# Optimization experiments

Measured on AMD Instinct MI355X. Metric: run time of the kernel, lower is better.

## Reference

```python
import jax, jax.numpy as jnp
import numpy as np

N, E, G, IN, H, L, C = 20000, 320000, 128, 16, 64, 4, 10
AVG_D_LOG = float(np.log(17.0))  # log(avg_degree + 1)


def setup_inputs() -> dict:
    key = jax.random.key(0)
    ks = jax.random.split(key, 24)
    p = lambda k, shape: jax.random.normal(k, shape, dtype=jnp.float32) * 0.05
    return dict(
        h=jax.random.normal(ks[0], (N, IN), jnp.float32),
        snorm_n=jax.random.uniform(ks[1], (N, 1), jnp.float32, 0.05, 1.0),
        embW=p(ks[2], (IN, H)), embB=p(ks[3], (H,)),
        preW=p(ks[4], (L, 2 * H, H)), preB=p(ks[5], (L, H)),
        postW=p(ks[6], (L, 13 * H, H)), postB=p(ks[7], (L, H)),
        mixW=p(ks[8], (L, H, H)), mixB=p(ks[9], (L, H)),
        r1W=p(ks[10], (H, H // 2)), r1B=p(ks[11], (H // 2,)),
        r2W=p(ks[12], (H // 2, H // 4)), r2B=p(ks[13], (H // 4,)),
        r3W=p(ks[14], (H // 4, C)), r3B=p(ks[15], (C,)),
        src=jax.random.randint(ks[16], (E,), 0, N),
        dst=jax.random.randint(ks[17], (E,), 0, N),
        graph_ids=jnp.sort(jax.random.randint(ks[18], (N,), 0, G)),
    )


def _pna_forward(h, snorm_n, embW, embB, preW, preB, postW, postB, mixW, mixB,
                 r1W, r1B, r2W, r2B, r3W, r3B, src, dst, graph_ids):
    # Degree-based scalers (computed once; graph is fixed across layers)
    deg = jax.ops.segment_sum(jnp.ones((E,), h.dtype), dst, num_segments=N)  # [N]
    degc = jnp.maximum(deg, 1.0)[:, None]
    logd = jnp.log(deg + 1.0)
    amp = (logd / AVG_D_LOG)[:, None]                      # amplification scaler
    att = (AVG_D_LOG / jnp.maximum(logd, 1e-5))[:, None]   # attenuation scaler
    has_nb = (deg > 0.0)[:, None]

    x = h @ embW + embB  # node embedding [N, H]
    for i in range(L):
        x_in = x
        # pretrans: per-edge message from cat(h_src, h_dst)  [E, H]
        m = jnp.concatenate([x[src], x[dst]], axis=-1) @ preW[i] + preB[i]
        # multi-aggregator reduce at dst: mean, max, min, std
        mean = jax.ops.segment_sum(m, dst, num_segments=N) / degc
        msq = jax.ops.segment_sum(m * m, dst, num_segments=N) / degc
        std = jnp.sqrt(jax.nn.relu(msq - mean * mean) + 1e-5)
        mx = jnp.where(has_nb, jax.ops.segment_max(m, dst, num_segments=N), 0.0)
        mn = jnp.where(has_nb, jax.ops.segment_min(m, dst, num_segments=N), 0.0)
        agg = jnp.concatenate([mean, mx, mn, std], axis=-1)  # [N, 4H]
        # degree scalers: identity, amplification, attenuation -> [N, 12H]
        scaled = jnp.concatenate([agg, agg * amp, agg * att], axis=-1)
        # posttrans over cat(scaled_agg, h) -> [N, H]
        y = jnp.concatenate([scaled, x], axis=-1) @ postW[i] + postB[i]
        # tower mixing network (LeakyReLU FC)
        y = jax.nn.leaky_relu(y @ mixW[i] + mixB[i])
        y = y * snorm_n          # graph norm
        x = x_in + y             # residual
    # mean-nodes readout per graph
    gsum = jax.ops.segment_sum(x, graph_ids, num_segments=G)
    cnt = jnp.maximum(jax.ops.segment_sum(jnp.ones((N,), x.dtype), graph_ids, num_segments=G), 1.0)
    hg = gsum / cnt[:, None]
    # MLPReadout: two halving ReLU layers + classifier
    hg = jax.nn.relu(hg @ r1W + r1B)
    hg = jax.nn.relu(hg @ r2W + r2B)
    return hg @ r3W + r3B  # [G, C]


def reference(h, snorm_n, embW, embB, preW, preB, postW, postB, mixW, mixB,
              r1W, r1B, r2W, r2B, r3W, r3B, src, dst, graph_ids):
    return _pna_forward(h, snorm_n, embW, embB, preW, preB, postW, postB,
                        mixW, mixB, r1W, r1B, r2W, r2B, r3W, r3B,
                        src, dst, graph_ids)
```

## Files before the change

### kernel.cpp

```cpp
#include <hip/hip_runtime.h>
#include <math.h>

#define N_ 20000
#define E_ 320000
#define G_ 128
#define IN_ 16
#define H_ 64
#define L_ 4
#define C_ 10
#define AVG_D_LOG 2.8332133440562162f

union F4 { float4 v; float f[4]; };

typedef _Float16 h8 __attribute__((ext_vector_type(8)));
typedef _Float16 h4 __attribute__((ext_vector_type(4)));
typedef float f4x __attribute__((ext_vector_type(4)));
#define MFMA16(a, b, c) __builtin_amdgcn_mfma_f32_16x16x32_f16((a), (b), (c), 0, 0, 0)


__global__ __launch_bounds__(256) void k_setup(
    const float* __restrict__ h, const float* __restrict__ embW, const float* __restrict__ embB,
    float* __restrict__ x,
    const float* __restrict__ preW, const float* __restrict__ postW, const float* __restrict__ mixW,
    _Float16* __restrict__ preWT, _Float16* __restrict__ postWT, _Float16* __restrict__ mixWT,
    int* __restrict__ zbase) {
  int bb = blockIdx.x, tid = threadIdx.x;
  if (bb < 5000) {
    int n = bb * 4 + (tid >> 6);
    int c = tid & 63;
    float acc = embB[c];
#pragma unroll
    for (int k = 0; k < IN_; k++) acc += h[n * IN_ + k] * embW[k * H_ + c];
    x[n * H_ + c] = acc;
  } else if (bb < 6024) {
    int idx = (bb - 5000) * 256 + tid;
    if (idx < 32768) {
      int l = idx >> 13, r = idx & 8191;
      int c = r >> 6, k = r & 63;
      preWT[idx] = (_Float16)preW[l * 8192 + k * 64 + c];
    } else if (idx < 245760) {
      int j = idx - 32768;
      int l = j / 53248, r = j % 53248;
      int c = r / 832, k = r % 832;
      postWT[j] = (_Float16)postW[l * 53248 + k * 64 + c];
    } else {
      int j = idx - 245760;
      int l = j >> 12, r = j & 4095;
      int c = r >> 6, k = r & 63;
      mixWT[j] = (_Float16)mixW[l * 4096 + k * 64 + c];
    }
  } else {
    int i = (bb - 6024) * 256 + tid;
    if (i < 2 * N_) zbase[i] = 0;
  }
}


__global__ __launch_bounds__(256) void k_hist(const int* __restrict__ dst, int* __restrict__ deg) {
  int e = blockIdx.x * 256 + threadIdx.x;
  if (e < E_) atomicAdd(&deg[dst[e]], 1);
}

__global__ __launch_bounds__(1024) void k_scan(const int* __restrict__ deg, int* __restrict__ offs,
    float* __restrict__ ampv, float* __restrict__ attv,
    float* __restrict__ invd, float* __restrict__ hnb) {
  __shared__ int sh[1024];
  int t = threadIdx.x;
  int base = t * 20;
  int local[20];
  int s = 0;
#pragma unroll
  for (int i = 0; i < 20; i++) {
    int idx = base + i;
    int v = (idx < N_) ? deg[idx] : 0;
    local[i] = s; s += v;
  }
  sh[t] = s;
  __syncthreads();
  for (int off = 1; off < 1024; off <<= 1) {
    int v = (t >= off) ? sh[t - off] : 0;
    __syncthreads();
    sh[t] += v;
    __syncthreads();
  }
  int excl = sh[t] - s;
#pragma unroll
  for (int i = 0; i < 20; i++) {
    int idx = base + i;
    if (idx < N_) offs[idx] = excl + local[i];
  }
  if (t == 0) offs[N_] = sh[1023];
  for (int idx = t; idx < N_; idx += 1024) {
    float d = (float)deg[idx];
    float logd = logf(d + 1.f);
    ampv[idx] = logd / AVG_D_LOG;
    attv[idx] = AVG_D_LOG / fmaxf(logd, 1e-5f);
    invd[idx] = 1.f / fmaxf(d, 1.f);
    hnb[idx] = d > 0.f ? 1.f : 0.f;
  }
}

__global__ __launch_bounds__(256) void k_scatter(const int* __restrict__ src, const int* __restrict__ dst,
    const int* __restrict__ offs, int* __restrict__ cursor, int* __restrict__ csr) {
  int e = blockIdx.x * 256 + threadIdx.x;
  if (e < E_) {
    int d = dst[e];
    int pos = offs[d] + atomicAdd(&cursor[d], 1);
    csr[pos] = src[e];
  }
}


__global__ __launch_bounds__(256) void k_pretrans(const float* __restrict__ x,
    const _Float16* __restrict__ WT, const float* __restrict__ Bv,
    _Float16* __restrict__ ah, float* __restrict__ b) {
  int tid = threadIdx.x;
  int n0 = blockIdx.x * 32;
  int lane = tid & 63, wv = tid >> 6;
  int mt = wv & 1, nh = wv >> 1;
  int l15 = lane & 15, k0q = (lane >> 4) * 8;
  int mrow = n0 + mt * 16 + l15;
  const float* xr = x + (size_t)mrow * 64;
  const _Float16* wb0 = WT + (size_t)(nh * 64 + l15) * 64 + k0q;
  f4x acc0 = {0.f,0.f,0.f,0.f}, acc1 = {0.f,0.f,0.f,0.f}, acc2 = {0.f,0.f,0.f,0.f}, acc3 = {0.f,0.f,0.f,0.f};
#pragma unroll
  for (int kb = 0; kb < 64; kb += 32) {
    int ko = kb + k0q;
    F4 xa, xb2;
    xa.v = *(const float4*)(xr + ko);
    xb2.v = *(const float4*)(xr + ko + 4);
    h8 af;
    af[0]=(_Float16)xa.f[0]; af[1]=(_Float16)xa.f[1]; af[2]=(_Float16)xa.f[2]; af[3]=(_Float16)xa.f[3];
    af[4]=(_Float16)xb2.f[0]; af[5]=(_Float16)xb2.f[1]; af[6]=(_Float16)xb2.f[2]; af[7]=(_Float16)xb2.f[3];
    acc0 = MFMA16(af, *(const h8*)(wb0 + kb), acc0);
    acc1 = MFMA16(af, *(const h8*)(wb0 + 1024 + kb), acc1);
    acc2 = MFMA16(af, *(const h8*)(wb0 + 2048 + kb), acc2);
    acc3 = MFMA16(af, *(const h8*)(wb0 + 3072 + kb), acc3);
  }
  int rbase = n0 + mt * 16 + (lane >> 4) * 4;
  f4x accs[4] = {acc0, acc1, acc2, acc3};
#pragma unroll
  for (int t = 0; t < 4; t++) {
    int col = nh * 64 + t * 16 + l15;
#pragma unroll
    for (int r = 0; r < 4; r++) {
      int n = rbase + r;
      if (col < 64) ah[(size_t)n * 64 + col] = (_Float16)accs[t][r];
      else          b[(size_t)n * 64 + (col - 64)] = accs[t][r] + Bv[col - 64];
    }
  }
}


__global__ __launch_bounds__(256) void k_layer(
    const _Float16* __restrict__ ahin, const float* __restrict__ bin,
    const int* __restrict__ offs, const int* __restrict__ csr,
    const float* __restrict__ invd, const float* __restrict__ hnb,
    const _Float16* __restrict__ WT, const float* __restrict__ Bv,
    const _Float16* __restrict__ mixWT, const float* __restrict__ mixB,
    const float* __restrict__ ampv, const float* __restrict__ attv,
    const float* __restrict__ snorm, float* __restrict__ x,
    const _Float16* __restrict__ preWT, const float* __restrict__ preB,
    _Float16* __restrict__ ahout, float* __restrict__ bout, int do_pre) {
  __shared__ _Float16 aggs[32 * 272];
  __shared__ _Float16 ys[32 * 80];
  __shared__ _Float16 xs[32 * 80];
  int tid = threadIdx.x;
  int n0 = blockIdx.x * 32;
  int lane = tid & 63, wv = tid >> 6;

  {
    int nl = tid >> 3, q = tid & 7;
    int n = n0 + nl;
    int o0 = offs[n];
    int deg = offs[n + 1] - o0;
    float sum[8], sq[8], mx[8], mn[8];
#pragma unroll
    for (int i = 0; i < 8; i++) {
      sum[i] = 0.f; sq[i] = 0.f;
      mx[i] = -__builtin_inff(); mn[i] = __builtin_inff();
    }
    int j = 0;
    for (; j + 3 < deg; j += 4) {
      int s0 = csr[o0 + j];
      int s1 = csr[o0 + j + 1];
      int s2 = csr[o0 + j + 2];
      int s3 = csr[o0 + j + 3];
      h8 a0 = *(const h8*)(ahin + (size_t)s0 * 64 + q * 8);
      h8 a1 = *(const h8*)(ahin + (size_t)s1 * 64 + q * 8);
      h8 a2 = *(const h8*)(ahin + (size_t)s2 * 64 + q * 8);
      h8 a3 = *(const h8*)(ahin + (size_t)s3 * 64 + q * 8);
#pragma unroll
      for (int i = 0; i < 8; i++) {
        float v0 = (float)a0[i], v1 = (float)a1[i], v2 = (float)a2[i], v3 = (float)a3[i];
        sum[i] += (v0 + v1) + (v2 + v3);
        sq[i] += v0 * v0;
        sq[i] += v1 * v1;
        sq[i] += v2 * v2;
        sq[i] += v3 * v3;
        mx[i] = fmaxf(mx[i], fmaxf(fmaxf(v0, v1), fmaxf(v2, v3)));
        mn[i] = fminf(mn[i], fminf(fminf(v0, v1), fminf(v2, v3)));
      }
    }
    for (; j < deg; j++) {
      int s0 = csr[o0 + j];
      h8 a0 = *(const h8*)(ahin + (size_t)s0 * 64 + q * 8);
#pragma unroll
      for (int i = 0; i < 8; i++) {
        float v0 = (float)a0[i];
        sum[i] += v0;
        sq[i] += v0 * v0;
        mx[i] = fmaxf(mx[i], v0);
        mn[i] = fminf(mn[i], v0);
      }
    }
    float inv = invd[n], hn = hnb[n];
    F4 b0v, b1v;
    b0v.v = *(const float4*)(bin + (size_t)n * 64 + q * 8);
    b1v.v = *(const float4*)(bin + (size_t)n * 64 + q * 8 + 4);
    float bf[8] = {b0v.f[0], b0v.f[1], b0v.f[2], b0v.f[3], b1v.f[0], b1v.f[1], b1v.f[2], b1v.f[3]};
    h8 hm, hx, hmn, hs;
#pragma unroll
    for (int i = 0; i < 8; i++) {
      float mean_a = sum[i] * inv;
      float var = sq[i] * inv - mean_a * mean_a;
      hs[i] = (_Float16)sqrtf(fmaxf(var, 0.f) + 1e-5f);
      bool nb = hn > 0.5f;
      hm[i] = (_Float16)(nb ? (mean_a + bf[i]) : 0.f);
      hx[i] = (_Float16)(nb ? (mx[i] + bf[i]) : 0.f);
      hmn[i] = (_Float16)(nb ? (mn[i] + bf[i]) : 0.f);
    }
    _Float16* ap = aggs + nl * 272 + q * 8;
    *(h8*)(ap) = hm;
    *(h8*)(ap + 64) = hx;
    *(h8*)(ap + 128) = hmn;
    *(h8*)(ap + 192) = hs;
  }
  __syncthreads();

  int mt = wv & 1, nh = wv >> 1;
  int l15 = lane & 15, k0q = (lane >> 4) * 8;
  int mrow = n0 + mt * 16 + l15;
  const _Float16* ag = aggs + (size_t)(mt * 16 + l15) * 272 + k0q;
  int col0 = nh * 32 + l15;
  const _Float16* w0 = WT + (size_t)col0 * 832 + k0q;
  const _Float16* w1 = w0 + (size_t)16 * 832;
  f4x aI0={0.f,0.f,0.f,0.f}, aI1={0.f,0.f,0.f,0.f};
  f4x aA0={0.f,0.f,0.f,0.f}, aA1={0.f,0.f,0.f,0.f};
  f4x aT0={0.f,0.f,0.f,0.f}, aT1={0.f,0.f,0.f,0.f};
#pragma unroll 4
  for (int kb = 0; kb < 256; kb += 32) {
    h8 af = *(const h8*)(ag + kb);
    aI0 = MFMA16(af, *(const h8*)(w0 + kb), aI0);
    aI1 = MFMA16(af, *(const h8*)(w1 + kb), aI1);
    aA0 = MFMA16(af, *(const h8*)(w0 + 256 + kb), aA0);
    aA1 = MFMA16(af, *(const h8*)(w1 + 256 + kb), aA1);
    aT0 = MFMA16(af, *(const h8*)(w0 + 512 + kb), aT0);
    aT1 = MFMA16(af, *(const h8*)(w1 + 512 + kb), aT1);
  }
  const float* xr = x + (size_t)mrow * 64;
#pragma unroll
  for (int kb = 0; kb < 64; kb += 32) {
    int ko = kb + k0q;
    F4 xa, xb2;
    xa.v = *(const float4*)(xr + ko);
    xb2.v = *(const float4*)(xr + ko + 4);
    h8 af;
    af[0]=(_Float16)xa.f[0]; af[1]=(_Float16)xa.f[1]; af[2]=(_Float16)xa.f[2]; af[3]=(_Float16)xa.f[3];
    af[4]=(_Float16)xb2.f[0]; af[5]=(_Float16)xb2.f[1]; af[6]=(_Float16)xb2.f[2]; af[7]=(_Float16)xb2.f[3];
    aI0 = MFMA16(af, *(const h8*)(w0 + 768 + kb), aI0);
    aI1 = MFMA16(af, *(const h8*)(w1 + 768 + kb), aI1);
  }
  int qr = (lane >> 4) * 4;
  int rbase = n0 + mt * 16 + qr;
  int yrow = mt * 16 + qr;
  float b0 = Bv[col0], b1 = Bv[col0 + 16];
#pragma unroll
  for (int r = 0; r < 4; r++) {
    int n = rbase + r;
    float amp = ampv[n], att = attv[n];
    ys[(yrow + r) * 80 + col0]      = (_Float16)(aI0[r] + b0 + amp * aA0[r] + att * aT0[r]);
    ys[(yrow + r) * 80 + col0 + 16] = (_Float16)(aI1[r] + b1 + amp * aA1[r] + att * aT1[r]);
  }
  __syncthreads();
  f4x m0 = {0.f,0.f,0.f,0.f}, m1 = {0.f,0.f,0.f,0.f};
  const _Float16* yr = ys + (size_t)(mt * 16 + l15) * 80 + k0q;
  const _Float16* mw0 = mixWT + (size_t)col0 * 64 + k0q;
  const _Float16* mw1 = mw0 + 16 * 64;
#pragma unroll
  for (int kb = 0; kb < 64; kb += 32) {
    h8 af = *(const h8*)(yr + kb);
    m0 = MFMA16(af, *(const h8*)(mw0 + kb), m0);
    m1 = MFMA16(af, *(const h8*)(mw1 + kb), m1);
  }
  float mb0 = mixB[col0], mb1 = mixB[col0 + 16];
#pragma unroll
  for (int r = 0; r < 4; r++) {
    int n = rbase + r;
    float sn = snorm[n];
    float t0 = m0[r] + mb0; t0 = t0 > 0.f ? t0 : 0.01f * t0;
    float t1 = m1[r] + mb1; t1 = t1 > 0.f ? t1 : 0.01f * t1;
    float* xp = x + (size_t)n * 64;
    float xo0 = xp[col0] + t0 * sn;
    float xo1 = xp[col0 + 16] + t1 * sn;
    xp[col0] = xo0;
    xp[col0 + 16] = xo1;
    xs[(yrow + r) * 80 + col0]      = (_Float16)xo0;
    xs[(yrow + r) * 80 + col0 + 16] = (_Float16)xo1;
  }

  if (do_pre) {
    __syncthreads();
    const _Float16* xf = xs + (size_t)(mt * 16 + l15) * 80 + k0q;
    const _Float16* wb0 = preWT + (size_t)(nh * 64 + l15) * 64 + k0q;
    f4x p0 = {0.f,0.f,0.f,0.f}, p1 = {0.f,0.f,0.f,0.f}, p2 = {0.f,0.f,0.f,0.f}, p3 = {0.f,0.f,0.f,0.f};
#pragma unroll
    for (int kb = 0; kb < 64; kb += 32) {
      h8 af = *(const h8*)(xf + kb);
      p0 = MFMA16(af, *(const h8*)(wb0 + kb), p0);
      p1 = MFMA16(af, *(const h8*)(wb0 + 1024 + kb), p1);
      p2 = MFMA16(af, *(const h8*)(wb0 + 2048 + kb), p2);
      p3 = MFMA16(af, *(const h8*)(wb0 + 3072 + kb), p3);
    }
    int prb = n0 + mt * 16 + (lane >> 4) * 4;
    f4x accs[4] = {p0, p1, p2, p3};
#pragma unroll
    for (int t = 0; t < 4; t++) {
      int col = nh * 64 + t * 16 + l15;
#pragma unroll
      for (int r = 0; r < 4; r++) {
        int n = prb + r;
        if (col < 64) ahout[(size_t)n * 64 + col] = (_Float16)accs[t][r];
        else          bout[(size_t)n * 64 + (col - 64)] = accs[t][r] + preB[col - 64];
      }
    }
  }
}


__device__ inline int lower_bound_gid(const int* __restrict__ gid, int val) {
  int lo = 0, hi = N_;
  while (lo < hi) {
    int mid = (lo + hi) >> 1;
    if (gid[mid] < val) lo = mid + 1; else hi = mid;
  }
  return lo;
}

__global__ __launch_bounds__(256) void k_readout_fused(
    const float* __restrict__ x, const int* __restrict__ gid,
    const float* __restrict__ r1W, const float* __restrict__ r1B,
    const float* __restrict__ r2W, const float* __restrict__ r2B,
    const float* __restrict__ r3W, const float* __restrict__ r3B,
    float* __restrict__ out) {
  __shared__ float part[4 * 64];
  __shared__ float hg[64];
  __shared__ float t1[32];
  __shared__ float t2[16];
  int g = blockIdx.x, tid = threadIdx.x;
  int lo = lower_bound_gid(gid, g);
  int hi = lower_bound_gid(gid, g + 1);
  int c = tid & 63, w = tid >> 6;
  float s = 0.f;
  for (int n = lo + w; n < hi; n += 4) s += x[(size_t)n * 64 + c];
  part[w * 64 + c] = s;
  __syncthreads();
  if (w == 0) {
    float tot = part[c] + part[64 + c] + part[128 + c] + part[192 + c];
    float cnt = (float)(hi - lo);
    if (cnt < 1.f) cnt = 1.f;
    hg[c] = tot / cnt;
  }
  __syncthreads();
  if (tid < 32) {
    float acc = r1B[tid];
#pragma unroll 8
    for (int k = 0; k < 64; k++) acc += hg[k] * r1W[k * 32 + tid];
    t1[tid] = fmaxf(acc, 0.f);
  }
  __syncthreads();
  if (tid < 16) {
    float acc = r2B[tid];
#pragma unroll 8
    for (int k = 0; k < 32; k++) acc += t1[k] * r2W[k * 16 + tid];
    t2[tid] = fmaxf(acc, 0.f);
  }
  __syncthreads();
  if (tid < 10) {
    float acc = r3B[tid];
#pragma unroll
    for (int k = 0; k < 16; k++) acc += t2[k] * r3W[k * 10 + tid];
    out[g * 10 + tid] = acc;
  }
}


extern "C" void kernel_launch(void* const* d_in, const int* in_sizes, int n_in,
                              void* d_out, int out_size, void* d_ws, size_t ws_size,
                              hipStream_t stream) {
  const float* h     = (const float*)d_in[0];
  const float* snorm = (const float*)d_in[1];
  const float* embW  = (const float*)d_in[2];
  const float* embB  = (const float*)d_in[3];
  const float* preW  = (const float*)d_in[4];
  const float* preB  = (const float*)d_in[5];
  const float* postW = (const float*)d_in[6];
  const float* postB = (const float*)d_in[7];
  const float* mixW  = (const float*)d_in[8];
  const float* mixB  = (const float*)d_in[9];
  const float* r1W   = (const float*)d_in[10];
  const float* r1B   = (const float*)d_in[11];
  const float* r2W   = (const float*)d_in[12];
  const float* r2B   = (const float*)d_in[13];
  const float* r3W   = (const float*)d_in[14];
  const float* r3B   = (const float*)d_in[15];
  const int* src     = (const int*)d_in[16];
  const int* dst     = (const int*)d_in[17];
  const int* gid     = (const int*)d_in[18];
  float* out = (float*)d_out;

  char* w = (char*)d_ws;
  float* x        = (float*)w; w += (size_t)N_ * 64 * 4;
  _Float16* ah0   = (_Float16*)w; w += (size_t)N_ * 64 * 2;
  _Float16* ah1   = (_Float16*)w; w += (size_t)N_ * 64 * 2;
  float* b0       = (float*)w; w += (size_t)N_ * 64 * 4;
  float* b1       = (float*)w; w += (size_t)N_ * 64 * 4;
  _Float16* preWT = (_Float16*)w; w += (size_t)4 * 128 * 64 * 2;
  _Float16* postWT= (_Float16*)w; w += (size_t)4 * 64 * 832 * 2;
  _Float16* mixWT = (_Float16*)w; w += (size_t)4 * 64 * 64 * 2;
  float* ampv = (float*)w; w += (size_t)N_ * 4;
  float* attv = (float*)w; w += (size_t)N_ * 4;
  float* invd = (float*)w; w += (size_t)N_ * 4;
  float* hnb  = (float*)w; w += (size_t)N_ * 4;
  int* csr    = (int*)w;   w += (size_t)E_ * 4;
  int* offs   = (int*)w;   w += (size_t)(N_ + 64) * 4;
  int* zbase  = (int*)w;
  int* deg    = (int*)w;   w += (size_t)N_ * 4;
  int* cursor = (int*)w;   w += (size_t)N_ * 4;

  k_setup<<<6181, 256, 0, stream>>>(h, embW, embB, x, preW, postW, mixW,
                                    preWT, postWT, mixWT, zbase);
  k_hist<<<E_ / 256, 256, 0, stream>>>(dst, deg);
  k_scan<<<1, 1024, 0, stream>>>(deg, offs, ampv, attv, invd, hnb);
  k_scatter<<<E_ / 256, 256, 0, stream>>>(src, dst, offs, cursor, csr);
  int gb = N_ / 32;
  k_pretrans<<<gb, 256, 0, stream>>>(x, preWT, preB, ah0, b0);
  _Float16* ahs[2] = {ah0, ah1};
  float* bs[2] = {b0, b1};
  for (int l = 0; l < L_; l++) {
    int pin = l & 1, pout = 1 - pin;
    k_layer<<<gb, 256, 0, stream>>>(ahs[pin], bs[pin], offs, csr, invd, hnb,
                                    postWT + (size_t)l * 53248, postB + l * H_,
                                    mixWT + (size_t)l * 4096, mixB + l * H_,
                                    ampv, attv, snorm, x,
                                    preWT + (size_t)(l + 1 < L_ ? l + 1 : 0) * 8192,
                                    preB + (l + 1 < L_ ? l + 1 : 0) * H_,
                                    ahs[pout], bs[pout], l + 1 < L_ ? 1 : 0);
  }
  k_readout_fused<<<G_, 256, 0, stream>>>(x, gid, r1W, r1B, r2W, r2B, r3W, r3B, out);
}
```

Baseline: 330.4 us.

## Double k_layer block to 512 threads, splitting gather and MFMA work finer

Launches the fused layer kernel with 512 threads per 32-node block instead of 256. In the gather phase each node is now handled by 16 threads reading 4 halfs each, and each of the 8 waves computes a 16-column slice of the posttrans, mix and pretrans GEMMs. This raises the number of memory requests in flight per CU during the irregular neighbour gather and lowers per-thread register use. In exchange it issues smaller 8-byte loads and keeps more waves waiting at the block barriers.

```diff
diff --git a/kernel.cpp b/kernel.cpp
--- a/kernel.cpp
+++ b/kernel.cpp
@@ -152,7 +152,7 @@
 }
 
 
-__global__ __launch_bounds__(256) void k_layer(
+__global__ __launch_bounds__(512) void k_layer(
     const _Float16* __restrict__ ahin, const float* __restrict__ bin,
     const int* __restrict__ offs, const int* __restrict__ csr,
     const float* __restrict__ invd, const float* __restrict__ hnb,
@@ -170,13 +170,13 @@
   int lane = tid & 63, wv = tid >> 6;
 
   {
-    int nl = tid >> 3, q = tid & 7;
+    int nl = tid >> 4, q = tid & 15;
     int n = n0 + nl;
     int o0 = offs[n];
     int deg = offs[n + 1] - o0;
-    float sum[8], sq[8], mx[8], mn[8];
-#pragma unroll
-    for (int i = 0; i < 8; i++) {
+    float sum[4], sq[4], mx[4], mn[4];
+#pragma unroll
+    for (int i = 0; i < 4; i++) {
       sum[i] = 0.f; sq[i] = 0.f;
       mx[i] = -__builtin_inff(); mn[i] = __builtin_inff();
     }
@@ -186,12 +186,12 @@
       int s1 = csr[o0 + j + 1];
       int s2 = csr[o0 + j + 2];
       int s3 = csr[o0 + j + 3];
-      h8 a0 = *(const h8*)(ahin + (size_t)s0 * 64 + q * 8);
-      h8 a1 = *(const h8*)(ahin + (size_t)s1 * 64 + q * 8);
-      h8 a2 = *(const h8*)(ahin + (size_t)s2 * 64 + q * 8);
-      h8 a3 = *(const h8*)(ahin + (size_t)s3 * 64 + q * 8);
-#pragma unroll
-      for (int i = 0; i < 8; i++) {
+      h4 a0 = *(const h4*)(ahin + (size_t)s0 * 64 + q * 4);
+      h4 a1 = *(const h4*)(ahin + (size_t)s1 * 64 + q * 4);
+      h4 a2 = *(const h4*)(ahin + (size_t)s2 * 64 + q * 4);
+      h4 a3 = *(const h4*)(ahin + (size_t)s3 * 64 + q * 4);
+#pragma unroll
+      for (int i = 0; i < 4; i++) {
         float v0 = (float)a0[i], v1 = (float)a1[i], v2 = (float)a2[i], v3 = (float)a3[i];
         sum[i] += (v0 + v1) + (v2 + v3);
         sq[i] += v0 * v0;
@@ -204,9 +204,9 @@
     }
     for (; j < deg; j++) {
       int s0 = csr[o0 + j];
-      h8 a0 = *(const h8*)(ahin + (size_t)s0 * 64 + q * 8);
-#pragma unroll
-      for (int i = 0; i < 8; i++) {
+      h4 a0 = *(const h4*)(ahin + (size_t)s0 * 64 + q * 4);
+#pragma unroll
+      for (int i = 0; i < 4; i++) {
         float v0 = (float)a0[i];
         sum[i] += v0;
         sq[i] += v0 * v0;
@@ -215,26 +215,23 @@
       }
     }
     float inv = invd[n], hn = hnb[n];
-    F4 b0v, b1v;
-    b0v.v = *(const float4*)(bin + (size_t)n * 64 + q * 8);
-    b1v.v = *(const float4*)(bin + (size_t)n * 64 + q * 8 + 4);
-    float bf[8] = {b0v.f[0], b0v.f[1], b0v.f[2], b0v.f[3], b1v.f[0], b1v.f[1], b1v.f[2], b1v.f[3]};
-    h8 hm, hx, hmn, hs;
-#pragma unroll
-    for (int i = 0; i < 8; i++) {
+    F4 bv; bv.v = *(const float4*)(bin + (size_t)n * 64 + q * 4);
+    h4 hm, hx, hmn, hs;
+#pragma unroll
+    for (int i = 0; i < 4; i++) {
       float mean_a = sum[i] * inv;
       float var = sq[i] * inv - mean_a * mean_a;
       hs[i] = (_Float16)sqrtf(fmaxf(var, 0.f) + 1e-5f);
       bool nb = hn > 0.5f;
-      hm[i] = (_Float16)(nb ? (mean_a + bf[i]) : 0.f);
-      hx[i] = (_Float16)(nb ? (mx[i] + bf[i]) : 0.f);
-      hmn[i] = (_Float16)(nb ? (mn[i] + bf[i]) : 0.f);
-    }
-    _Float16* ap = aggs + nl * 272 + q * 8;
-    *(h8*)(ap) = hm;
-    *(h8*)(ap + 64) = hx;
-    *(h8*)(ap + 128) = hmn;
-    *(h8*)(ap + 192) = hs;
+      hm[i] = (_Float16)(nb ? (mean_a + bv.f[i]) : 0.f);
+      hx[i] = (_Float16)(nb ? (mx[i] + bv.f[i]) : 0.f);
+      hmn[i] = (_Float16)(nb ? (mn[i] + bv.f[i]) : 0.f);
+    }
+    _Float16* ap = aggs + nl * 272 + q * 4;
+    *(h4*)(ap) = hm;
+    *(h4*)(ap + 64) = hx;
+    *(h4*)(ap + 128) = hmn;
+    *(h4*)(ap + 192) = hs;
   }
   __syncthreads();
 
@@ -242,21 +239,15 @@
   int l15 = lane & 15, k0q = (lane >> 4) * 8;
   int mrow = n0 + mt * 16 + l15;
   const _Float16* ag = aggs + (size_t)(mt * 16 + l15) * 272 + k0q;
-  int col0 = nh * 32 + l15;
+  int col0 = nh * 16 + l15;
   const _Float16* w0 = WT + (size_t)col0 * 832 + k0q;
-  const _Float16* w1 = w0 + (size_t)16 * 832;
-  f4x aI0={0.f,0.f,0.f,0.f}, aI1={0.f,0.f,0.f,0.f};
-  f4x aA0={0.f,0.f,0.f,0.f}, aA1={0.f,0.f,0.f,0.f};
-  f4x aT0={0.f,0.f,0.f,0.f}, aT1={0.f,0.f,0.f,0.f};
+  f4x aI = {0.f,0.f,0.f,0.f}, aA = {0.f,0.f,0.f,0.f}, aT = {0.f,0.f,0.f,0.f};
 #pragma unroll 4
   for (int kb = 0; kb < 256; kb += 32) {
     h8 af = *(const h8*)(ag + kb);
-    aI0 = MFMA16(af, *(const h8*)(w0 + kb), aI0);
-    aI1 = MFMA16(af, *(const h8*)(w1 + kb), aI1);
-    aA0 = MFMA16(af, *(const h8*)(w0 + 256 + kb), aA0);
-    aA1 = MFMA16(af, *(const h8*)(w1 + 256 + kb), aA1);
-    aT0 = MFMA16(af, *(const h8*)(w0 + 512 + kb), aT0);
-    aT1 = MFMA16(af, *(const h8*)(w1 + 512 + kb), aT1);
+    aI = MFMA16(af, *(const h8*)(w0 + kb), aI);
+    aA = MFMA16(af, *(const h8*)(w0 + 256 + kb), aA);
+    aT = MFMA16(af, *(const h8*)(w0 + 512 + kb), aT);
   }
   const float* xr = x + (size_t)mrow * 64;
 #pragma unroll
@@ -268,65 +259,56 @@
     h8 af;
     af[0]=(_Float16)xa.f[0]; af[1]=(_Float16)xa.f[1]; af[2]=(_Float16)xa.f[2]; af[3]=(_Float16)xa.f[3];
     af[4]=(_Float16)xb2.f[0]; af[5]=(_Float16)xb2.f[1]; af[6]=(_Float16)xb2.f[2]; af[7]=(_Float16)xb2.f[3];
-    aI0 = MFMA16(af, *(const h8*)(w0 + 768 + kb), aI0);
-    aI1 = MFMA16(af, *(const h8*)(w1 + 768 + kb), aI1);
+    aI = MFMA16(af, *(const h8*)(w0 + 768 + kb), aI);
   }
   int qr = (lane >> 4) * 4;
   int rbase = n0 + mt * 16 + qr;
   int yrow = mt * 16 + qr;
-  float b0 = Bv[col0], b1 = Bv[col0 + 16];
+  float b0 = Bv[col0];
 #pragma unroll
   for (int r = 0; r < 4; r++) {
     int n = rbase + r;
     float amp = ampv[n], att = attv[n];
-    ys[(yrow + r) * 80 + col0]      = (_Float16)(aI0[r] + b0 + amp * aA0[r] + att * aT0[r]);
-    ys[(yrow + r) * 80 + col0 + 16] = (_Float16)(aI1[r] + b1 + amp * aA1[r] + att * aT1[r]);
-  }
-  __syncthreads();
-  f4x m0 = {0.f,0.f,0.f,0.f}, m1 = {0.f,0.f,0.f,0.f};
+    ys[(yrow + r) * 80 + col0] = (_Float16)(aI[r] + b0 + amp * aA[r] + att * aT[r]);
+  }
+  __syncthreads();
+  f4x m0 = {0.f,0.f,0.f,0.f};
   const _Float16* yr = ys + (size_t)(mt * 16 + l15) * 80 + k0q;
   const _Float16* mw0 = mixWT + (size_t)col0 * 64 + k0q;
-  const _Float16* mw1 = mw0 + 16 * 64;
 #pragma unroll
   for (int kb = 0; kb < 64; kb += 32) {
     h8 af = *(const h8*)(yr + kb);
     m0 = MFMA16(af, *(const h8*)(mw0 + kb), m0);
-    m1 = MFMA16(af, *(const h8*)(mw1 + kb), m1);
-  }
-  float mb0 = mixB[col0], mb1 = mixB[col0 + 16];
+  }
+  float mb0 = mixB[col0];
 #pragma unroll
   for (int r = 0; r < 4; r++) {
     int n = rbase + r;
     float sn = snorm[n];
     float t0 = m0[r] + mb0; t0 = t0 > 0.f ? t0 : 0.01f * t0;
-    float t1 = m1[r] + mb1; t1 = t1 > 0.f ? t1 : 0.01f * t1;
     float* xp = x + (size_t)n * 64;
     float xo0 = xp[col0] + t0 * sn;
-    float xo1 = xp[col0 + 16] + t1 * sn;
     xp[col0] = xo0;
-    xp[col0 + 16] = xo1;
-    xs[(yrow + r) * 80 + col0]      = (_Float16)xo0;
-    xs[(yrow + r) * 80 + col0 + 16] = (_Float16)xo1;
+    xs[(yrow + r) * 80 + col0] = (_Float16)xo0;
   }
 
   if (do_pre) {
     __syncthreads();
+    int ch = wv >> 1;
     const _Float16* xf = xs + (size_t)(mt * 16 + l15) * 80 + k0q;
-    const _Float16* wb0 = preWT + (size_t)(nh * 64 + l15) * 64 + k0q;
-    f4x p0 = {0.f,0.f,0.f,0.f}, p1 = {0.f,0.f,0.f,0.f}, p2 = {0.f,0.f,0.f,0.f}, p3 = {0.f,0.f,0.f,0.f};
+    const _Float16* wb0 = preWT + (size_t)(ch * 32 + l15) * 64 + k0q;
+    f4x p0 = {0.f,0.f,0.f,0.f}, p1 = {0.f,0.f,0.f,0.f};
 #pragma unroll
     for (int kb = 0; kb < 64; kb += 32) {
       h8 af = *(const h8*)(xf + kb);
       p0 = MFMA16(af, *(const h8*)(wb0 + kb), p0);
       p1 = MFMA16(af, *(const h8*)(wb0 + 1024 + kb), p1);
-      p2 = MFMA16(af, *(const h8*)(wb0 + 2048 + kb), p2);
-      p3 = MFMA16(af, *(const h8*)(wb0 + 3072 + kb), p3);
     }
     int prb = n0 + mt * 16 + (lane >> 4) * 4;
-    f4x accs[4] = {p0, p1, p2, p3};
-#pragma unroll
-    for (int t = 0; t < 4; t++) {
-      int col = nh * 64 + t * 16 + l15;
+    f4x accs[2] = {p0, p1};
+#pragma unroll
+    for (int t = 0; t < 2; t++) {
+      int col = ch * 32 + t * 16 + l15;
 #pragma unroll
       for (int r = 0; r < 4; r++) {
         int n = prb + r;
@@ -449,7 +431,7 @@
   float* bs[2] = {b0, b1};
   for (int l = 0; l < L_; l++) {
     int pin = l & 1, pout = 1 - pin;
-    k_layer<<<gb, 256, 0, stream>>>(ahs[pin], bs[pin], offs, csr, invd, hnb,
+    k_layer<<<gb, 512, 0, stream>>>(ahs[pin], bs[pin], offs, csr, invd, hnb,
                                     postWT + (size_t)l * 53248, postB + l * H_,
                                     mixWT + (size_t)l * 4096, mixB + l * H_,
                                     ampv, attv, snorm, x,
```

Measured after the change: 330.0 us. About the same (-0.1%).
